# Optimization experiments

Hardware: AMD Instinct MI355X
Metric: run time of the kernel (lower is better)

Reference implementation:

```python
import jax, jax.numpy as jnp
import numpy as np

B, S, D = 2, 2048, 2048
H = 16
Q_LORA = 1024
KV_LORA = 512
NOPE = 128
ROPE = 64
VH = 128
QK = NOPE + ROPE
EPS = 1e-3
SCALE = QK ** -0.5


def rms_norm(x, w):
    x32 = x.astype(jnp.float32)
    n = x32 * jax.lax.rsqrt(jnp.mean(x32 * x32, axis=-1, keepdims=True) + EPS)
    return w * n.astype(x.dtype)


def apply_rope(x, cos, sin):
    # x: [b, s, h, d]; cos/sin: [1, s, 1, d//2].
    # torch view_as_complex pairs consecutive elements: (x0,x1),(x2,x3),...
    xr, xi = x[..., 0::2], x[..., 1::2]
    yr = xr * cos - xi * sin
    yi = xr * sin + xi * cos
    return jnp.stack([yr, yi], axis=-1).reshape(x.shape)


def setup_inputs() -> dict:
    key = jax.random.key(0)
    ks = jax.random.split(key, 8)

    def lin(k, out, inn):
        bound = 1.0 / float(np.sqrt(inn))
        return jax.random.uniform(k, (out, inn), jnp.float32, -bound, bound)

    inv_freq = 1.0 / (10000.0 ** (np.arange(0, ROPE, 2, dtype=np.float32) / ROPE))
    ang = np.arange(S, dtype=np.float32)[:, None] * inv_freq[None, :]  # [S, ROPE/2]
    return {
        "x": jax.random.normal(ks[0], (B, S, D), jnp.float32),
        "start_pos": 0,
        "cos": jnp.asarray(np.cos(ang), jnp.float32),
        "sin": jnp.asarray(np.sin(ang), jnp.float32),
        "wq_a_w": lin(ks[1], Q_LORA, D),
        "wq_a_b": jnp.zeros((Q_LORA,), jnp.float32),
        "q_norm_w": jnp.ones((Q_LORA,), jnp.float32),
        "wq_b_w": lin(ks[2], H * QK, Q_LORA),
        "wq_b_b": jnp.zeros((H * QK,), jnp.float32),
        "wkv_a_w": lin(ks[3], KV_LORA + ROPE, D),
        "wkv_a_b": jnp.zeros((KV_LORA + ROPE,), jnp.float32),
        "kv_norm_w": jnp.ones((KV_LORA,), jnp.float32),
        "wkv_b_w": lin(ks[4], H * (NOPE + VH), KV_LORA),
        "wo_w": lin(ks[5], D, H * VH),
        "wo_b": jnp.zeros((D,), jnp.float32),
    }


def reference(x, start_pos, cos, sin, wq_a_w, wq_a_b, q_norm_w, wq_b_w, wq_b_b,
              wkv_a_w, wkv_a_b, kv_norm_w, wkv_b_w, wo_w, wo_b):
    b, s, _ = x.shape
    cos_ = cos[None, :, None, :]
    sin_ = sin[None, :, None, :]

    # q path: low-rank down-proj, RMSNorm, up-proj
    q = rms_norm(x @ wq_a_w.T + wq_a_b, q_norm_w) @ wq_b_w.T + wq_b_b
    q = q.reshape(b, s, H, QK)
    q_nope, q_pe = q[..., :NOPE], q[..., NOPE:]
    q_pe = apply_rope(q_pe, cos_, sin_)

    # kv path: joint low-rank latent + rope key
    kv_full = x @ wkv_a_w.T + wkv_a_b
    kv, k_pe = kv_full[..., :KV_LORA], kv_full[..., KV_LORA:]
    k_pe = apply_rope(k_pe[:, :, None, :], cos_, sin_)[:, :, 0, :]  # [b, t, ROPE]

    wkv_b = wkv_b_w.reshape(H, NOPE + VH, KV_LORA)
    # absorb k up-projection into q (MLA trick): q_nope -> latent space
    q_nope = jnp.einsum('bshd,hdc->bshc', q_nope, wkv_b[:, :NOPE])  # [b,s,H,KV_LORA]

    kv_c = rms_norm(kv, kv_norm_w)  # latent KV cache contents [b, t, KV_LORA]

    scores = (jnp.einsum('bshc,btc->bsht', q_nope, kv_c)
              + jnp.einsum('bshr,btr->bsht', q_pe, k_pe)) * SCALE
    # NOTE: source builds a causal mask but never adds it -> plain softmax (faithful)
    probs = jax.nn.softmax(scores.astype(jnp.float32), axis=-1).astype(x.dtype)

    o = jnp.einsum('bsht,btc->bshc', probs, kv_c)          # latent output
    o = jnp.einsum('bshc,hdc->bshd', o, wkv_b[:, NOPE:])    # v up-projection
    return o.reshape(b, s, H * VH) @ wo_w.T + wo_b
```

## Files before the change

### kernel.cpp

```cpp
#include <hip/hip_runtime.h>
#include <stdint.h>

typedef uint16_t u16;
typedef __bf16 bf16x8 __attribute__((ext_vector_type(8)));
typedef float f32x4 __attribute__((ext_vector_type(4)));
typedef u16 u16x8 __attribute__((ext_vector_type(8)));

#define EPS 1e-3f
#define SCALE_F 0.07216878364870323f
#define THR_RAW 110.0f

__device__ __forceinline__ float bf2f(u16 u) {
    union { uint32_t i; float f; } v; v.i = ((uint32_t)u) << 16; return v.f;
}
__device__ __forceinline__ u16 f2bf(float f) {
    union { float f; uint32_t i; } v; v.f = f;
    uint32_t x = v.i;
    return (u16)((x + 0x7fffu + ((x >> 16) & 1u)) >> 16);
}

__device__ __forceinline__ void async_cp16(const u16* g, u16* l) {
    __builtin_amdgcn_global_load_lds(
        (const __attribute__((address_space(1))) uint32_t*)g,
        (__attribute__((address_space(3))) uint32_t*)l,
        16, 0, 0);
}

struct Cvt {
    const void* src[14];
    u16* dst[14];
    long off[15];
};

__global__ __launch_bounds__(256) void cvt_kernel(Cvt c, const uint32_t* qnw_u32, long total8)
{
    const long i8 = (long)blockIdx.x * 256 + threadIdx.x;
    if (i8 >= total8) return;
    const long e = i8 * 8;
    const bool is_f32 = (qnw_u32[0] == 0x3F800000u);
    int t = 0;
    while (e >= c.off[t + 1]) ++t;
    const long local = e - c.off[t];
    u16* d = c.dst[t] + local;
    if (is_f32) {
        const float* s = (const float*)c.src[t] + local;
        #pragma unroll
        for (int j = 0; j < 8; ++j) d[j] = f2bf(s[j]);
    } else {
        const u16* s = (const u16*)c.src[t] + local;
        #pragma unroll
        for (int j = 0; j < 8; ++j) d[j] = s[j];
    }
}

__global__ __launch_bounds__(256) void gemm_bt_kernel(
    const u16* __restrict__ A, const u16* __restrict__ B,
    const u16* __restrict__ bias, u16* __restrict__ C,
    int M, int N, int K, int lda, int ldb, int ldc, float alpha, int c_f32,
    int z0, int hcnt,
    long sAl, long sAb, long sAh,
    long sBl, long sBb, long sBh,
    long sCl, long sCb, long sCh)
{
    const int zl = blockIdx.z;
    const int zg = z0 + zl;
    const int zb = zg / hcnt, zh = zg - zb * hcnt;
    A += (long)zl * sAl + (long)zb * sAb + (long)zh * sAh;
    B += (long)zl * sBl + (long)zb * sBb + (long)zh * sBh;
    C += (long)zl * sCl + (long)zb * sCb + (long)zh * sCh;

    __shared__ u16 As[128 * 64];
    __shared__ u16 Bs[128 * 64];

    const int tid  = threadIdx.x;
    const int wave = tid >> 6, lane = tid & 63;
    const int wm = (wave >> 1) << 6, wn = (wave & 1) << 6;
    const int quad = lane >> 4, r15 = lane & 15;

    const int tileM = blockIdx.y * 128;
    const int tileN = blockIdx.x * 128;

    const u16* Ag[4]; const u16* Bg[4];
    u16* lA[4]; u16* lB[4];
    #pragma unroll
    for (int i = 0; i < 4; ++i) {
        const int cc = i * 256 + tid;
        const int rA = cc >> 3, kb = (cc & 7) << 3;
        int rB = tileN + rA; if (rB > N - 1) rB = N - 1;
        Ag[i] = A + (long)(tileM + rA) * lda + kb;
        Bg[i] = B + (long)rB * ldb + kb;
        lA[i] = &As[cc << 3];
        lB[i] = &Bs[cc << 3];
    }

    f32x4 acc[4][4] = {};

    const u16* aRd[4]; const u16* bRd[4];
    #pragma unroll
    for (int i = 0; i < 4; ++i) {
        aRd[i] = &As[(wm + i * 16 + r15) * 64 + quad * 8];
        bRd[i] = &Bs[(wn + i * 16 + r15) * 64 + quad * 8];
    }

    for (int k0 = 0; k0 < K; k0 += 64) {
        #pragma unroll
        for (int i = 0; i < 4; ++i) {
            async_cp16(Ag[i], lA[i]);
            async_cp16(Bg[i], lB[i]);
            Ag[i] += 64; Bg[i] += 64;
        }
        __syncthreads();
        #pragma unroll
        for (int kk = 0; kk < 2; ++kk) {
            bf16x8 af[4], bfr[4];
            #pragma unroll
            for (int i = 0; i < 4; ++i) {
                af[i]  = *(const bf16x8*)(aRd[i] + kk * 32);
                bfr[i] = *(const bf16x8*)(bRd[i] + kk * 32);
            }
            #pragma unroll
            for (int mi = 0; mi < 4; ++mi)
                #pragma unroll
                for (int ni = 0; ni < 4; ++ni)
                    acc[mi][ni] = __builtin_amdgcn_mfma_f32_16x16x32_bf16(
                        af[mi], bfr[ni], acc[mi][ni], 0, 0, 0);
        }
        __syncthreads();
    }

    #pragma unroll
    for (int mi = 0; mi < 4; ++mi) {
        const int row = tileM + wm + mi * 16 + quad * 4;
        #pragma unroll
        for (int ni = 0; ni < 4; ++ni) {
            const int col = tileN + wn + ni * 16 + r15;
            if (col < N) {
                if (c_f32) {
                    const float bv = bias ? bf2f(bias[col]) : 0.f;
                    #pragma unroll
                    for (int r = 0; r < 4; ++r)
                        ((float*)C)[(long)(row + r) * ldc + col] =
                            acc[mi][ni][r] * alpha + bv;
                } else {
                    #pragma unroll
                    for (int r = 0; r < 4; ++r) {
                        u16 t = f2bf(acc[mi][ni][r] * alpha);
                        if (bias) t = f2bf(bf2f(t) + bf2f(bias[col]));
                        C[(long)(row + r) * ldc + col] = t;
                    }
                }
            }
        }
    }
}

#define PS 72

__global__ __launch_bounds__(256, 2) void flash_kernel(
    const u16* __restrict__ q, const u16* __restrict__ K2,
    const u16* __restrict__ Vt, u16* __restrict__ O,
    const u16* __restrict__ cosb, const u16* __restrict__ sinb)
{
    __shared__ __align__(16) u16 Ks[64 * 192];
    __shared__ __align__(16) u16 Vs[128 * 64];
    __shared__ __align__(16) u16 Ps[4][32 * PS];

    const int bid = blockIdx.x;
    const int xcd = bid & 7;
    const int idx = bid >> 3;
    const int bh  = xcd * 4 + (idx >> 4);
    const int mt  = idx & 15;
    const int b = bh >> 4, h = bh & 15;

    const int tid = threadIdx.x;
    const int wave = tid >> 6, lane = tid & 63;
    const int quad = lane >> 4, r15 = lane & 15;
    const int r7 = r15 & 7;

    const long qrow0 = (long)b * 2048 + mt * 128 + wave * 32;
    u16* myPs = Ps[wave];

    bf16x8 qf[2][6];
    #pragma unroll
    for (int mi = 0; mi < 2; ++mi) {
        const u16* qp = q + (qrow0 + mi * 16 + r15) * 3072 + h * 192 + quad * 8;
        #pragma unroll
        for (int kst = 0; kst < 4; ++kst)
            qf[mi][kst] = *(const bf16x8*)(qp + kst * 32);
        const int srow = mt * 128 + wave * 32 + mi * 16 + r15;
        #pragma unroll
        for (int kst = 4; kst < 6; ++kst) {
            const u16x8 v = *(const u16x8*)(qp + kst * 32);
            u16x8 o;
            const int jj0 = (kst - 4) * 16 + quad * 4;
            #pragma unroll
            for (int pp = 0; pp < 4; ++pp) {
                const float xr = bf2f(v[2 * pp]), xi = bf2f(v[2 * pp + 1]);
                const float c  = bf2f(cosb[(long)srow * 32 + jj0 + pp]);
                const float si = bf2f(sinb[(long)srow * 32 + jj0 + pp]);
                o[2 * pp]     = f2bf(bf2f(f2bf(xr * c))  - bf2f(f2bf(xi * si)));
                o[2 * pp + 1] = f2bf(bf2f(f2bf(xr * si)) + bf2f(f2bf(xi * c)));
            }
            qf[mi][kst] = *(const bf16x8*)&o;
        }
    }

    f32x4 Oacc[2][8] = {};
    float m_i[2][4], l_i[2][4];
    #pragma unroll
    for (int mi = 0; mi < 2; ++mi)
        #pragma unroll
        for (int r = 0; r < 4; ++r) { m_i[mi][r] = -1e30f; l_i[mi][r] = 0.f; }

    const u16* Kbh = K2 + (long)b * 2048 * 3072 + h * 192;
    const u16* Vbh = Vt + (long)bh * 128 * 2048;

    const u16* gK[6];
    #pragma unroll
    for (int i = 0; i < 6; ++i) {
        const int c = i * 256 + tid;
        const int row = c / 24, s = c - row * 24;
        gK[i] = Kbh + (long)row * 3072 + ((s ^ (row & 7)) << 3);
    }
    const u16* gV[4];
    #pragma unroll
    for (int i = 0; i < 4; ++i) {
        const int c = i * 256 + tid;
        const int d = c >> 3, s = c & 7;
        gV[i] = Vbh + (long)d * 2048 + ((s ^ (d & 7)) << 3);
    }

    #pragma unroll
    for (int i = 0; i < 6; ++i) {
        async_cp16(gK[i], &Ks[(i * 256 + tid) << 3]);
        gK[i] += 64 * 3072;
    }
    __syncthreads();

    for (int j = 0; j < 32; ++j) {
        #pragma unroll
        for (int i = 0; i < 4; ++i) {
            async_cp16(gV[i], &Vs[(i * 256 + tid) << 3]);
            gV[i] += 64;
        }

        f32x4 S[2][4] = {};
        __builtin_amdgcn_s_setprio(1);
        #pragma unroll
        for (int kst = 0; kst < 6; ++kst) {
            bf16x8 bfr[4];
            #pragma unroll
            for (int ni = 0; ni < 4; ++ni)
                bfr[ni] = *(const bf16x8*)&Ks[(ni * 16 + r15) * 192
                                              + (((kst * 4 + quad) ^ r7) << 3)];
            #pragma unroll
            for (int mi = 0; mi < 2; ++mi)
                #pragma unroll
                for (int ni = 0; ni < 4; ++ni)
                    S[mi][ni] = __builtin_amdgcn_mfma_f32_16x16x32_bf16(
                        qf[mi][kst], bfr[ni], S[mi][ni], 0, 0, 0);
        }
        __builtin_amdgcn_s_setprio(0);

        __syncthreads();

        #pragma unroll
        for (int i = 0; i < 6; ++i) {
            async_cp16(gK[i], &Ks[(i * 256 + tid) << 3]);
            gK[i] += 64 * 3072;
        }

        float tmax[2][4];
        float gmax = -1e30f;
        #pragma unroll
        for (int mi = 0; mi < 2; ++mi)
            #pragma unroll
            for (int r = 0; r < 4; ++r) {
                float t = S[mi][0][r];
                #pragma unroll
                for (int ni = 1; ni < 4; ++ni) t = fmaxf(t, S[mi][ni][r]);
                t = fmaxf(t, __shfl_xor(t, 1, 16));
                t = fmaxf(t, __shfl_xor(t, 2, 16));
                t = fmaxf(t, __shfl_xor(t, 4, 16));
                t = fmaxf(t, __shfl_xor(t, 8, 16));
                tmax[mi][r] = t;
                gmax = fmaxf(gmax, t - m_i[mi][r]);
            }
        if (!__all(gmax <= THR_RAW)) {
            #pragma unroll
            for (int mi = 0; mi < 2; ++mi)
                #pragma unroll
                for (int r = 0; r < 4; ++r) {
                    const float mnew = fmaxf(m_i[mi][r], tmax[mi][r]);
                    const float al = __expf((m_i[mi][r] - mnew) * SCALE_F);
                    m_i[mi][r] = mnew;
                    l_i[mi][r] *= al;
                    #pragma unroll
                    for (int ni = 0; ni < 8; ++ni) Oacc[mi][ni][r] *= al;
                }
        }
        #pragma unroll
        for (int mi = 0; mi < 2; ++mi)
            #pragma unroll
            for (int r = 0; r < 4; ++r) {
                const int lrow = mi * 16 + quad * 4 + r;
                const float mm = m_i[mi][r];
                float ps = 0.f;
                #pragma unroll
                for (int ni = 0; ni < 4; ++ni) {
                    const float pv = __expf((S[mi][ni][r] - mm) * SCALE_F);
                    ps += pv;
                    myPs[lrow * PS + ni * 16 + r15] = f2bf(pv);
                }
                ps += __shfl_xor(ps, 1, 16);
                ps += __shfl_xor(ps, 2, 16);
                ps += __shfl_xor(ps, 4, 16);
                ps += __shfl_xor(ps, 8, 16);
                l_i[mi][r] += ps;
            }

        __builtin_amdgcn_s_setprio(1);
        #pragma unroll
        for (int kst = 0; kst < 2; ++kst) {
            bf16x8 af[2], bv[8];
            #pragma unroll
            for (int mi = 0; mi < 2; ++mi)
                af[mi] = *(const bf16x8*)&myPs[(mi * 16 + r15) * PS
                                               + kst * 32 + quad * 8];
            #pragma unroll
            for (int ni = 0; ni < 8; ++ni)
                bv[ni] = *(const bf16x8*)&Vs[(ni * 16 + r15) * 64
                                             + (((kst * 4 + quad) ^ r7) << 3)];
            #pragma unroll
            for (int mi = 0; mi < 2; ++mi)
                #pragma unroll
                for (int ni = 0; ni < 8; ++ni)
                    Oacc[mi][ni] = __builtin_amdgcn_mfma_f32_16x16x32_bf16(
                        af[mi], bv[ni], Oacc[mi][ni], 0, 0, 0);
        }
        __builtin_amdgcn_s_setprio(0);

        __syncthreads();
    }

    #pragma unroll
    for (int mi = 0; mi < 2; ++mi)
        #pragma unroll
        for (int r = 0; r < 4; ++r) {
            const float inv = 1.f / l_i[mi][r];
            const long row = qrow0 + mi * 16 + quad * 4 + r;
            #pragma unroll
            for (int ni = 0; ni < 8; ++ni)
                O[row * 2048 + h * 128 + ni * 16 + r15] =
                    f2bf(Oacc[mi][ni][r] * inv);
        }
}

__global__ __launch_bounds__(256) void rmsnorm_kernel(
    const u16* __restrict__ x, const u16* __restrict__ w, u16* __restrict__ y,
    int n, int ldx)
{
    const long row = blockIdx.x;
    const u16* xr = x + row * ldx;
    u16* yr = y + row * ldx;
    const int tid = threadIdx.x;
    const int cnt = n >> 8;
    float v[4];
    float ss = 0.f;
    for (int i = 0; i < cnt; ++i) { v[i] = bf2f(xr[tid + (i << 8)]); ss += v[i] * v[i]; }
    for (int o = 32; o; o >>= 1) ss += __shfl_xor(ss, o, 64);
    __shared__ float sm[4];
    if ((tid & 63) == 0) sm[tid >> 6] = ss;
    __syncthreads();
    const float rinv = rsqrtf((sm[0] + sm[1] + sm[2] + sm[3]) / (float)n + EPS);
    for (int i = 0; i < cnt; ++i) {
        const u16 nb = f2bf(v[i] * rinv);
        yr[tid + (i << 8)] = f2bf(bf2f(w[tid + (i << 8)]) * bf2f(nb));
    }
}

__global__ __launch_bounds__(256) void kv_kernel(
    const u16* __restrict__ cosb, const u16* __restrict__ sinb,
    const u16* __restrict__ w, u16* __restrict__ comb, u16* __restrict__ K2)
{
    const long bs = blockIdx.x;
    const int s = (int)(bs & 2047);
    u16* io = comb + bs * 1600 + 1024;
    const int tid = threadIdx.x;
    const float v0 = bf2f(io[tid * 2]), v1 = bf2f(io[tid * 2 + 1]);
    float ss = v0 * v0 + v1 * v1;
    for (int off = 32; off; off >>= 1) ss += __shfl_xor(ss, off, 64);
    __shared__ float sm[4];
    __shared__ u16 rp[64];
    if ((tid & 63) == 0) sm[tid >> 6] = ss;
    __syncthreads();
    const float rinv = rsqrtf((sm[0] + sm[1] + sm[2] + sm[3]) / 512.f + EPS);
    const u16 n0 = f2bf(v0 * rinv), n1 = f2bf(v1 * rinv);
    io[tid * 2]     = f2bf(bf2f(w[tid * 2]) * bf2f(n0));
    io[tid * 2 + 1] = f2bf(bf2f(w[tid * 2 + 1]) * bf2f(n1));
    if (tid < 32) {
        const int j = tid;
        const float xr = bf2f(io[512 + 2 * j]), xi = bf2f(io[512 + 2 * j + 1]);
        const float c = bf2f(cosb[s * 32 + j]), si = bf2f(sinb[s * 32 + j]);
        rp[2 * j]     = f2bf(bf2f(f2bf(xr * c))  - bf2f(f2bf(xi * si)));
        rp[2 * j + 1] = f2bf(bf2f(f2bf(xr * si)) + bf2f(f2bf(xi * c)));
    }
    __syncthreads();
    #pragma unroll
    for (int i = 0; i < 4; ++i) {
        const int slot = tid + (i << 8);
        const int h = slot >> 6, r = slot & 63;
        K2[bs * 3072 + h * 192 + 128 + r] = rp[r];
    }
}

extern "C" void kernel_launch(void* const* d_in, const int* in_sizes, int n_in,
                              void* d_out, int out_size, void* d_ws, size_t ws_size,
                              hipStream_t stream)
{
    float* out = (float*)d_out;

    char* p = (char*)d_ws;
    auto alloc = [&](size_t elems) { u16* r = (u16*)p; p += elems * 2; return r; };
    u16* c_cos  = alloc(65536);
    u16* c_sin  = alloc(65536);
    u16* c_wqa  = alloc(2097152);
    u16* c_wkva = alloc(1179648);
    u16* c_wqab = alloc(1024);
    u16* c_wkvab= alloc(576);
    u16* c_qnw  = alloc(1024);
    u16* c_wqb  = alloc(3145728);
    u16* c_wqbb = alloc(3072);
    u16* c_kvnw = alloc(512);
    u16* c_wkvb = alloc(2097152);
    u16* c_wo   = alloc(4194304);
    u16* c_wob  = alloc(2048);
    u16* q    = alloc(4096UL * 3072);
    u16* K2   = alloc(4096UL * 3072);
    u16* O    = alloc(4096UL * 2048);
    u16* comb = alloc(4096UL * 1600);
    u16* xb = (u16*)d_out;
    u16* Vt = (u16*)d_out + 8388608;

    Cvt cv;
    const long sizes[14] = {8388608, 65536, 65536, 2097152, 1024, 1024, 3145728,
                            3072, 1179648, 576, 512, 2097152, 4194304, 2048};
    u16* dsts[14] = {xb, c_cos, c_sin, c_wqa, c_wqab, c_qnw, c_wqb, c_wqbb,
                     c_wkva, c_wkvab, c_kvnw, c_wkvb, c_wo, c_wob};
    const int srcidx[14] = {0, 2, 3, 4, 5, 6, 7, 8, 9, 10, 11, 12, 13, 14};
    long acc_off = 0;
    for (int t = 0; t < 14; ++t) {
        cv.src[t] = d_in[srcidx[t]];
        cv.dst[t] = dsts[t];
        cv.off[t] = acc_off;
        acc_off += sizes[t];
    }
    cv.off[14] = acc_off;
    const long total8 = acc_off / 8;
    cvt_kernel<<<dim3((unsigned)((total8 + 255) / 256)), dim3(256), 0, stream>>>(
        cv, (const uint32_t*)d_in[6], total8);

    auto gemm = [&](const u16* A, const u16* B, const u16* bias, u16* C,
                    int M, int N, int K, int lda, int ldb, int ldc, float alpha,
                    int c_f32, int nz, int z0, int hcnt,
                    long sAl, long sAb, long sAh,
                    long sBl, long sBb, long sBh,
                    long sCl, long sCb, long sCh) {
        dim3 grid((N + 127) / 128, M / 128, nz);
        gemm_bt_kernel<<<grid, dim3(256), 0, stream>>>(
            A, B, bias, C, M, N, K, lda, ldb, ldc, alpha, c_f32, z0, hcnt,
            sAl, sAb, sAh, sBl, sBb, sBh, sCl, sCb, sCh);
    };

    gemm(xb, c_wqa, c_wqab, comb, 4096, 1600, 2048, 2048, 2048, 1600, 1.f, 0,
         1, 0, 1, 0, 0, 0, 0, 0, 0, 0, 0, 0);
    rmsnorm_kernel<<<4096, 256, 0, stream>>>(comb, c_qnw, comb, 1024, 1600);
    gemm(comb, c_wqb, c_wqbb, q, 4096, 3072, 1024, 1600, 1024, 3072, 1.f, 0,
         1, 0, 1, 0, 0, 0, 0, 0, 0, 0, 0, 0);
    kv_kernel<<<4096, 256, 0, stream>>>(c_cos, c_sin, c_kvnw, comb, K2);
    gemm(comb + 1024, c_wkvb, nullptr, K2, 4096, 128, 512, 1600, 512, 3072, 1.f, 0,
         16, 0, 16, 0, 0, 0, 0, 0, 256L * 512, 0, 0, 192);
    gemm(c_wkvb + 128 * 512, comb + 1024, nullptr, Vt, 128, 2048, 512, 512, 1600, 2048,
         1.f, 0,
         32, 0, 16,
         0, 0, 256L * 512,
         0, 2048L * 1600, 0,
         0, 16L * 128 * 2048, 128L * 2048);
    flash_kernel<<<dim3(512), dim3(256), 0, stream>>>(q, K2, Vt, O, c_cos, c_sin);
    gemm(O, c_wo, c_wob, (u16*)out, 4096, 2048, 2048, 2048, 2048, 2048, 1.f, 1,
         1, 0, 1, 0, 0, 0, 0, 0, 0, 0, 0, 0);
}
```

Before: 529.8 us.

## Merge K and V up-projection GEMMs into one launch, vectorize convert, use exp2

Combines the K-absorb and V-transpose batched GEMMs into a single dual-problem kernel that dispatches blocks by flat index, removing one launch and letting the two small grids share the GPU. The fp32-to-bf16 convert kernel now uses 16-byte vector loads and stores instead of scalar element accesses. The flash softmax uses exp2f with a log2e-prefolded scale, and the max reduction is rewritten as a tree. Flat-index decoding adds some integer arithmetic per block, and exp2f may round slightly differently from __expf.

```diff
diff --git a/kernel.cpp b/kernel.cpp
--- a/kernel.cpp
+++ b/kernel.cpp
@@ -8,6 +8,7 @@
 
 #define EPS 1e-3f
 #define SCALE_F 0.07216878364870323f
+#define SCALE_L2E 0.104117546f
 #define THR_RAW 110.0f
 
 __device__ __forceinline__ float bf2f(u16 u) {
@@ -44,41 +45,45 @@
     u16* d = c.dst[t] + local;
     if (is_f32) {
         const float* s = (const float*)c.src[t] + local;
-        #pragma unroll
-        for (int j = 0; j < 8; ++j) d[j] = f2bf(s[j]);
+        const f32x4 a = *(const f32x4*)s;
+        const f32x4 b = *(const f32x4*)(s + 4);
+        u16x8 o;
+        #pragma unroll
+        for (int j = 0; j < 4; ++j) { o[j] = f2bf(a[j]); o[j + 4] = f2bf(b[j]); }
+        *(u16x8*)d = o;
     } else {
-        const u16* s = (const u16*)c.src[t] + local;
-        #pragma unroll
-        for (int j = 0; j < 8; ++j) d[j] = s[j];
-    }
-}
-
-__global__ __launch_bounds__(256) void gemm_bt_kernel(
-    const u16* __restrict__ A, const u16* __restrict__ B,
-    const u16* __restrict__ bias, u16* __restrict__ C,
-    int M, int N, int K, int lda, int ldb, int ldc, float alpha, int c_f32,
-    int z0, int hcnt,
-    long sAl, long sAb, long sAh,
-    long sBl, long sBb, long sBh,
-    long sCl, long sCb, long sCh)
-{
-    const int zl = blockIdx.z;
-    const int zg = z0 + zl;
-    const int zb = zg / hcnt, zh = zg - zb * hcnt;
-    A += (long)zl * sAl + (long)zb * sAb + (long)zh * sAh;
-    B += (long)zl * sBl + (long)zb * sBb + (long)zh * sBh;
-    C += (long)zl * sCl + (long)zb * sCb + (long)zh * sCh;
-
-    __shared__ u16 As[128 * 64];
-    __shared__ u16 Bs[128 * 64];
+        *(u16x8*)d = *(const u16x8*)((const u16*)c.src[t] + local);
+    }
+}
+
+struct GemmP {
+    const u16* A; const u16* B; const u16* bias; u16* C;
+    int M, N, K, lda, ldb, ldc; float alpha; int c_f32;
+    int z0, hcnt;
+    long sAl, sAb, sAh, sBl, sBb, sBh, sCl, sCb, sCh;
+    int gx, gy;
+};
+
+__device__ __forceinline__ void gemm_body(
+    u16* As, u16* Bs, int bx, int by, int bz, const GemmP& p)
+{
+    const u16* A = p.A; const u16* B = p.B; const u16* bias = p.bias;
+    u16* C = p.C;
+    const int N = p.N, K = p.K, lda = p.lda, ldb = p.ldb, ldc = p.ldc;
+
+    const int zg = p.z0 + bz;
+    const int zb = zg / p.hcnt, zh = zg - zb * p.hcnt;
+    A += (long)bz * p.sAl + (long)zb * p.sAb + (long)zh * p.sAh;
+    B += (long)bz * p.sBl + (long)zb * p.sBb + (long)zh * p.sBh;
+    C += (long)bz * p.sCl + (long)zb * p.sCb + (long)zh * p.sCh;
 
     const int tid  = threadIdx.x;
     const int wave = tid >> 6, lane = tid & 63;
     const int wm = (wave >> 1) << 6, wn = (wave & 1) << 6;
     const int quad = lane >> 4, r15 = lane & 15;
 
-    const int tileM = blockIdx.y * 128;
-    const int tileN = blockIdx.x * 128;
+    const int tileM = by * 128;
+    const int tileN = bx * 128;
 
     const u16* Ag[4]; const u16* Bg[4];
     u16* lA[4]; u16* lB[4];
@@ -135,22 +140,44 @@
         for (int ni = 0; ni < 4; ++ni) {
             const int col = tileN + wn + ni * 16 + r15;
             if (col < N) {
-                if (c_f32) {
+                if (p.c_f32) {
                     const float bv = bias ? bf2f(bias[col]) : 0.f;
                     #pragma unroll
                     for (int r = 0; r < 4; ++r)
                         ((float*)C)[(long)(row + r) * ldc + col] =
-                            acc[mi][ni][r] * alpha + bv;
+                            acc[mi][ni][r] * p.alpha + bv;
                 } else {
                     #pragma unroll
                     for (int r = 0; r < 4; ++r) {
-                        u16 t = f2bf(acc[mi][ni][r] * alpha);
+                        u16 t = f2bf(acc[mi][ni][r] * p.alpha);
                         if (bias) t = f2bf(bf2f(t) + bf2f(bias[col]));
                         C[(long)(row + r) * ldc + col] = t;
                     }
                 }
             }
         }
+    }
+}
+
+__global__ __launch_bounds__(256) void gemm_bt_kernel(GemmP p)
+{
+    __shared__ u16 As[128 * 64];
+    __shared__ u16 Bs[128 * 64];
+    gemm_body(As, Bs, blockIdx.x, blockIdx.y, blockIdx.z, p);
+}
+
+__global__ __launch_bounds__(256) void gemm_dual_kernel(GemmP pa, GemmP pb, int na)
+{
+    __shared__ u16 As[128 * 64];
+    __shared__ u16 Bs[128 * 64];
+    int bid = blockIdx.x;
+    if (bid < na) {
+        const int bx = bid % pa.gx; const int rem = bid / pa.gx;
+        gemm_body(As, Bs, bx, rem % pa.gy, rem / pa.gy, pa);
+    } else {
+        bid -= na;
+        const int bx = bid % pb.gx; const int rem = bid / pb.gx;
+        gemm_body(As, Bs, bx, rem % pb.gy, rem / pb.gy, pb);
     }
 }
 
@@ -276,9 +303,8 @@
         for (int mi = 0; mi < 2; ++mi)
             #pragma unroll
             for (int r = 0; r < 4; ++r) {
-                float t = S[mi][0][r];
-                #pragma unroll
-                for (int ni = 1; ni < 4; ++ni) t = fmaxf(t, S[mi][ni][r]);
+                float t = fmaxf(fmaxf(S[mi][0][r], S[mi][1][r]),
+                                fmaxf(S[mi][2][r], S[mi][3][r]));
                 t = fmaxf(t, __shfl_xor(t, 1, 16));
                 t = fmaxf(t, __shfl_xor(t, 2, 16));
                 t = fmaxf(t, __shfl_xor(t, 4, 16));
@@ -292,7 +318,7 @@
                 #pragma unroll
                 for (int r = 0; r < 4; ++r) {
                     const float mnew = fmaxf(m_i[mi][r], tmax[mi][r]);
-                    const float al = __expf((m_i[mi][r] - mnew) * SCALE_F);
+                    const float al = exp2f((m_i[mi][r] - mnew) * SCALE_L2E);
                     m_i[mi][r] = mnew;
                     l_i[mi][r] *= al;
                     #pragma unroll
@@ -308,7 +334,7 @@
                 float ps = 0.f;
                 #pragma unroll
                 for (int ni = 0; ni < 4; ++ni) {
-                    const float pv = __expf((S[mi][ni][r] - mm) * SCALE_F);
+                    const float pv = exp2f((S[mi][ni][r] - mm) * SCALE_L2E);
                     ps += pv;
                     myPs[lrow * PS + ni * 16 + r15] = f2bf(pv);
                 }
@@ -460,33 +486,47 @@
     cvt_kernel<<<dim3((unsigned)((total8 + 255) / 256)), dim3(256), 0, stream>>>(
         cv, (const uint32_t*)d_in[6], total8);
 
-    auto gemm = [&](const u16* A, const u16* B, const u16* bias, u16* C,
-                    int M, int N, int K, int lda, int ldb, int ldc, float alpha,
-                    int c_f32, int nz, int z0, int hcnt,
-                    long sAl, long sAb, long sAh,
-                    long sBl, long sBb, long sBh,
-                    long sCl, long sCb, long sCh) {
-        dim3 grid((N + 127) / 128, M / 128, nz);
-        gemm_bt_kernel<<<grid, dim3(256), 0, stream>>>(
-            A, B, bias, C, M, N, K, lda, ldb, ldc, alpha, c_f32, z0, hcnt,
-            sAl, sAb, sAh, sBl, sBb, sBh, sCl, sCb, sCh);
+    auto mkp = [&](const u16* A, const u16* B, const u16* bias, u16* C,
+                   int M, int N, int K, int lda, int ldb, int ldc, float alpha,
+                   int c_f32, int z0, int hcnt,
+                   long sAl, long sAb, long sAh,
+                   long sBl, long sBb, long sBh,
+                   long sCl, long sCb, long sCh) {
+        GemmP g;
+        g.A = A; g.B = B; g.bias = bias; g.C = C;
+        g.M = M; g.N = N; g.K = K; g.lda = lda; g.ldb = ldb; g.ldc = ldc;
+        g.alpha = alpha; g.c_f32 = c_f32; g.z0 = z0; g.hcnt = hcnt;
+        g.sAl = sAl; g.sAb = sAb; g.sAh = sAh;
+        g.sBl = sBl; g.sBb = sBb; g.sBh = sBh;
+        g.sCl = sCl; g.sCb = sCb; g.sCh = sCh;
+        g.gx = (N + 127) / 128; g.gy = M / 128;
+        return g;
     };
-
-    gemm(xb, c_wqa, c_wqab, comb, 4096, 1600, 2048, 2048, 2048, 1600, 1.f, 0,
-         1, 0, 1, 0, 0, 0, 0, 0, 0, 0, 0, 0);
+    auto gemm = [&](const GemmP& g, int nz) {
+        gemm_bt_kernel<<<dim3(g.gx, g.gy, nz), dim3(256), 0, stream>>>(g);
+    };
+
+    gemm(mkp(xb, c_wqa, c_wqab, comb, 4096, 1600, 2048, 2048, 2048, 1600, 1.f, 0,
+             0, 1, 0, 0, 0, 0, 0, 0, 0, 0, 0), 1);
     rmsnorm_kernel<<<4096, 256, 0, stream>>>(comb, c_qnw, comb, 1024, 1600);
-    gemm(comb, c_wqb, c_wqbb, q, 4096, 3072, 1024, 1600, 1024, 3072, 1.f, 0,
-         1, 0, 1, 0, 0, 0, 0, 0, 0, 0, 0, 0);
+    gemm(mkp(comb, c_wqb, c_wqbb, q, 4096, 3072, 1024, 1600, 1024, 3072, 1.f, 0,
+             0, 1, 0, 0, 0, 0, 0, 0, 0, 0, 0), 1);
     kv_kernel<<<4096, 256, 0, stream>>>(c_cos, c_sin, c_kvnw, comb, K2);
-    gemm(comb + 1024, c_wkvb, nullptr, K2, 4096, 128, 512, 1600, 512, 3072, 1.f, 0,
-         16, 0, 16, 0, 0, 0, 0, 0, 256L * 512, 0, 0, 192);
-    gemm(c_wkvb + 128 * 512, comb + 1024, nullptr, Vt, 128, 2048, 512, 512, 1600, 2048,
-         1.f, 0,
-         32, 0, 16,
-         0, 0, 256L * 512,
-         0, 2048L * 1600, 0,
-         0, 16L * 128 * 2048, 128L * 2048);
+    {
+        GemmP pk = mkp(comb + 1024, c_wkvb, nullptr, K2,
+                       4096, 128, 512, 1600, 512, 3072, 1.f, 0,
+                       0, 16, 0, 0, 0, 0, 0, 256L * 512, 0, 0, 192);
+        pk.gx = 1; pk.gy = 32;
+        GemmP pv = mkp(c_wkvb + 128 * 512, comb + 1024, nullptr, Vt,
+                       128, 2048, 512, 512, 1600, 2048, 1.f, 0,
+                       0, 16,
+                       0, 0, 256L * 512,
+                       0, 2048L * 1600, 0,
+                       0, 16L * 128 * 2048, 128L * 2048);
+        pv.gx = 16; pv.gy = 1;
+        gemm_dual_kernel<<<dim3(1024), dim3(256), 0, stream>>>(pk, pv, 512);
+    }
     flash_kernel<<<dim3(512), dim3(256), 0, stream>>>(q, K2, Vt, O, c_cos, c_sin);
-    gemm(O, c_wo, c_wob, (u16*)out, 4096, 2048, 2048, 2048, 2048, 2048, 1.f, 1,
-         1, 0, 1, 0, 0, 0, 0, 0, 0, 0, 0, 0);
-}
+    gemm(mkp(O, c_wo, c_wob, (u16*)out, 4096, 2048, 2048, 2048, 2048, 2048, 1.f, 1,
+             0, 1, 0, 0, 0, 0, 0, 0, 0, 0, 0), 1);
+}
```

Result: no change. 532.7 us (+0.5%).
